# Kernel optimization log

Measured on AMD Instinct MI355X. Metric: run time of the kernel, lower is better.

## Reference

```python
import jax, jax.numpy as jnp
import numpy as np

NMS_PRE, NMS_POST, NMS_THRESH = 1024, 512, 0.7
B, A, FEAT = 4, 70400, 27648
BN_EPS = 1e-5


def _bev_iou(boxes):
    # boxes: [K, 7] (x, y, z, dx, dy, dz, ry); axis-aligned BEV IoU
    x, y, dx, dy = boxes[:, 0], boxes[:, 1], boxes[:, 3], boxes[:, 4]
    x1, x2 = x - 0.5 * dx, x + 0.5 * dx
    y1, y2 = y - 0.5 * dy, y + 0.5 * dy
    iw = jnp.clip(jnp.minimum(x2[:, None], x2[None, :]) - jnp.maximum(x1[:, None], x1[None, :]), 0.0)
    ih = jnp.clip(jnp.minimum(y2[:, None], y2[None, :]) - jnp.maximum(y1[:, None], y1[None, :]), 0.0)
    inter = iw * ih
    area = dx * dy
    return inter / jnp.clip(area[:, None] + area[None, :] - inter, 1e-6)


def _greedy_nms(boxes, thresh):
    # boxes sorted by score desc; returns keep mask [K]
    K = boxes.shape[0]
    iou = _bev_iou(boxes)
    idx = jnp.arange(K)

    def step(keep, i):
        sup = (iou[i] > thresh) & (idx > i) & keep[i]
        return keep & ~sup, None

    keep, _ = jax.lax.scan(step, jnp.ones(K, dtype=bool), jnp.arange(K))
    return keep


def _proposal_one(box, cls):
    # box: [A, 7], cls: [A, n_cls]  ->  padded rois [NPOST,7], scores [NPOST], labels [NPOST]
    score = jnp.max(cls, axis=-1)
    label = jnp.argmax(cls, axis=-1)
    top_score, top_idx = jax.lax.top_k(score, NMS_PRE)
    top_box = box[top_idx]
    keep = _greedy_nms(top_box, NMS_THRESH)
    # stable: kept entries first, preserving score order
    order = jnp.argsort(jnp.where(keep, jnp.arange(NMS_PRE), NMS_PRE + jnp.arange(NMS_PRE)))
    sel = order[:NMS_POST]
    valid = jnp.arange(NMS_POST) < jnp.minimum(jnp.sum(keep), NMS_POST)
    rois = jnp.where(valid[:, None], top_box[sel], 0.0)
    roi_score = jnp.where(valid, top_score[sel], 0.0)
    roi_label = jnp.where(valid, label[top_idx][sel], 0) + 1  # +1 as in module
    return rois, roi_score, roi_label


def _bn_relu(h, g, b):
    # eval-mode BN with running_mean=0, running_var=1
    return jax.nn.relu(h * (g / jnp.sqrt(1.0 + BN_EPS)) + b)


def _decode(reg, anchors):
    # ResidualCoder_v1.decode_torch
    xa, ya, za = anchors[..., 0], anchors[..., 1], anchors[..., 2]
    dxa, dya, dza, ra = anchors[..., 3], anchors[..., 4], anchors[..., 5], anchors[..., 6]
    xt, yt, zt = reg[..., 0], reg[..., 1], reg[..., 2]
    dxt, dyt, dzt, rt = reg[..., 3], reg[..., 4], reg[..., 5], reg[..., 6]
    diag = jnp.sqrt(dxa * dxa + dya * dya)
    return jnp.stack([
        xt * diag + xa, yt * diag + ya, zt * dza + za,
        jnp.exp(dxt) * dxa, jnp.exp(dyt) * dya, jnp.exp(dzt) * dza,
        rt + ra], axis=-1)


def _rotate_z(box, ang):
    # rotate x,y of box [..., 7] by ang [...]
    c, s = jnp.cos(ang), jnp.sin(ang)
    x = box[..., 0] * c - box[..., 1] * s
    y = box[..., 0] * s + box[..., 1] * c
    return jnp.concatenate([x[..., None], y[..., None], box[..., 2:]], axis=-1)


def reference(rpn_box_preds, rpn_cls_preds, pooled_features,
              Ws1, g1, b1, Ws2, g2, b2,
              Wc1, gc1, bc1, Wc2, gc2, bc2, Wc3, bc3,
              Wr1, gr1, br1, Wr2, gr2, br2, Wr3, br3):
    # proposal_layer: per-batch topk + NMS + padded scatter (vmapped)
    rois, roi_scores, roi_labels = jax.vmap(_proposal_one)(rpn_box_preds, rpn_cls_preds)

    # shared / cls / reg heads (1x1 Conv1d == per-roi MLP), dropout off (eval)
    x = _bn_relu(pooled_features @ Ws1.T, g1, b1)
    x = _bn_relu(x @ Ws2.T, g2, b2)
    c = _bn_relu(x @ Wc1.T, gc1, bc1)
    c = _bn_relu(c @ Wc2.T, gc2, bc2)
    cls_preds = c @ Wc3.T + bc3          # [B*NPOST, 1]
    r = _bn_relu(x @ Wr1.T, gr1, br1)
    r = _bn_relu(r @ Wr2.T, gr2, br2)
    reg_preds = r @ Wr3.T + br3          # [B*NPOST, 7]

    bsz = rois.shape[0]
    cls_preds = cls_preds.reshape(bsz, -1, cls_preds.shape[-1])
    reg_preds = reg_preds.reshape(bsz, -1, 7)

    # generate_predict_box: decode against detached rois with xyz zeroed
    anchors = jax.lax.stop_gradient(rois)
    anchors = anchors.at[..., 0:3].set(0.0)
    box_ct = _decode(reg_preds, anchors)
    box_preds = _rotate_z(box_ct, rois[..., 6])
    box_preds = jnp.concatenate([box_preds[..., 0:3] + rois[..., 0:3], box_preds[..., 3:]], axis=-1)

    return jnp.concatenate([cls_preds, box_preds, roi_scores[..., None]], axis=-1)  # [B, NPOST, 9]


def setup_inputs():
    key = jax.random.key(0)
    ks = jax.random.split(key, 32)
    u = jax.random.uniform(ks[0], (B, A, 7), dtype=jnp.float32)
    lo = jnp.array([0.0, -40.0, -2.0, 1.5, 1.4, 1.0, -3.14159], jnp.float32)
    hi = jnp.array([70.0, 40.0, 0.0, 4.5, 2.0, 2.0, 3.14159], jnp.float32)
    rpn_box_preds = lo + u * (hi - lo)
    rpn_cls_preds = jax.random.normal(ks[1], (B, A, 3), dtype=jnp.float32)
    pooled_features = jax.random.normal(ks[2], (B * NMS_POST, FEAT), dtype=jnp.float32) * 0.1

    def w(k, o, i, std=None):
        s = (1.0 / np.sqrt(i)) if std is None else std
        return jax.random.normal(k, (o, i), dtype=jnp.float32) * s

    d = dict(
        rpn_box_preds=rpn_box_preds, rpn_cls_preds=rpn_cls_preds, pooled_features=pooled_features,
        Ws1=w(ks[3], 256, FEAT), g1=jnp.ones(256), b1=jnp.zeros(256),
        Ws2=w(ks[4], 256, 256), g2=jnp.ones(256), b2=jnp.zeros(256),
        Wc1=w(ks[5], 256, 256), gc1=jnp.ones(256), bc1=jnp.zeros(256),
        Wc2=w(ks[6], 256, 256), gc2=jnp.ones(256), bc2=jnp.zeros(256),
        Wc3=w(ks[7], 1, 256), bc3=jnp.zeros(1),
        Wr1=w(ks[8], 256, 256), gr1=jnp.ones(256), br1=jnp.zeros(256),
        Wr2=w(ks[9], 256, 256), gr2=jnp.ones(256), br2=jnp.zeros(256),
        Wr3=w(ks[10], 7, 256, std=0.001), br3=jnp.zeros(7),
    )
    return d
```

## Files before the change

kernel.cpp:

```cpp
#include <hip/hip_runtime.h>
#include <cstdint>

typedef unsigned int u32;
typedef unsigned long long u64;
typedef unsigned short u16;

#define BATCH 4
#define A_CNT 70400
#define FEAT 27648
#define KSPLIT 16
#define KCHUNK 1728
#define NTILE_IT 27

typedef __attribute__((ext_vector_type(8))) short bf16x8;
typedef __attribute__((ext_vector_type(4))) float f32x4;
typedef __attribute__((ext_vector_type(2))) u32 u32x2;
typedef __attribute__((ext_vector_type(4))) u32 u32x4;

constexpr size_t OF_KEYS = 0;
constexpr size_t OF_TBOX = OF_KEYS + 1126400;
constexpr size_t OF_TSC  = OF_TBOX + 114688;
constexpr size_t OF_BX1  = OF_TSC + 16384;
constexpr size_t OF_BX2  = OF_BX1 + 16384;
constexpr size_t OF_BY1  = OF_BX2 + 16384;
constexpr size_t OF_BY2  = OF_BY1 + 16384;
constexpr size_t OF_BAR  = OF_BY2 + 16384;
constexpr size_t OF_MASK = OF_BAR + 16384;
constexpr size_t OF_ROIS = OF_MASK + 524288;
constexpr size_t OF_RSC  = OF_ROIS + 57344;
constexpr size_t OF_BSW  = OF_RSC + 8192;
constexpr size_t OF_PART = OF_BSW + 14155776;
constexpr size_t WS_NEED = OF_PART + 33554432;

__device__ __forceinline__ u32 keyOf(float f) {
  u32 u = __float_as_uint(f);
  return (u & 0x80000000u) ? ~u : (u | 0x80000000u);
}
__device__ __forceinline__ float keyToF(u32 k) {
  u32 u = (k & 0x80000000u) ? (k ^ 0x80000000u) : ~k;
  return __uint_as_float(u);
}
__device__ __forceinline__ u16 f2bf(float f) {
  u32 u = __float_as_uint(f);
  u32 r = 0x7FFFu + ((u >> 16) & 1u);
  return (u16)((u + r) >> 16);
}
__device__ __forceinline__ void gload_lds16(const void* g, void* l) {
  auto gp = reinterpret_cast<const __attribute__((address_space(1))) unsigned int*>(
      reinterpret_cast<uintptr_t>(g));
  auto lp = reinterpret_cast<__attribute__((address_space(3))) unsigned int*>(
      reinterpret_cast<uintptr_t>(l));
  __builtin_amdgcn_global_load_lds(gp, lp, 16, 0, 0);
}
__device__ __forceinline__ u64 shflx64(u64 v, int m) {
  u32 lo = (u32)v, hi = (u32)(v >> 32);
  lo = __shfl_xor(lo, m, 64);
  hi = __shfl_xor(hi, m, 64);
  return ((u64)hi << 32) | lo;
}
__device__ __forceinline__ u32x4 pack8(float4 a, float4 b) {
  u32x4 o;
  o.x = (u32)f2bf(a.x) | ((u32)f2bf(a.y) << 16);
  o.y = (u32)f2bf(a.z) | ((u32)f2bf(a.w) << 16);
  o.z = (u32)f2bf(b.x) | ((u32)f2bf(b.y) << 16);
  o.w = (u32)f2bf(b.z) | ((u32)f2bf(b.w) << 16);
  return o;
}

__global__ __launch_bounds__(1024) void k_fatA(const float* __restrict__ cls,
    const float* __restrict__ Ws1, u32* __restrict__ keys, u32* __restrict__ Bsw)
{
  int bid = blockIdx.x;
  int t = threadIdx.x;
  if (bid < 864) {
    u32 w = (u32)bid * 1024u + t;
    u32 tile = w >> 11;
    u32 rem = w & 2047u;
    u32 n = rem >> 3;
    u32 pq = (rem & 7u) << 4;
    u32 q0 = pq ^ ((n & 7u) << 4);
    u32 col0 = tile * 64u + (q0 >> 1);
    const float* src = Ws1 + (size_t)n * FEAT + col0;
    float4 f0 = *(const float4*)src;
    float4 f1 = *(const float4*)(src + 4);
    ((u32x4*)Bsw)[w] = pack8(f0, f1);
    return;
  }
  u32 g = (u32)(bid - 864) * 1024u + t;
  float s0 = cls[(size_t)g * 3 + 0];
  float s1 = cls[(size_t)g * 3 + 1];
  float s2 = cls[(size_t)g * 3 + 2];
  keys[g] = keyOf(fmaxf(s0, fmaxf(s1, s2)));
}

__global__ __launch_bounds__(1024) void k_big(const u32* __restrict__ keys,
    const float* __restrict__ boxes, const float* __restrict__ A,
    const u32* __restrict__ Bsw, float* __restrict__ part,
    float* __restrict__ tbox, float* __restrict__ tsc,
    float* __restrict__ bx1, float* __restrict__ bx2, float* __restrict__ by1,
    float* __restrict__ by2, float* __restrict__ bar)
{
  __shared__ __align__(16) char smem[131072];
  int bid = blockIdx.x;
  int t = threadIdx.x;
  if (bid < 4) {
    int b = bid;
    int lane = t & 63, wv = t >> 6;
    const u32* kb = keys + (size_t)b * A_CNT;
    u64* s = (u64*)smem;
    u32* partials = (u32*)(smem + 16384);
    u32* ccp = (u32*)(smem + 16448);
    u32 h[35];
#pragma unroll
    for (int j = 0; j < 35; ++j) {
      int g0 = t + ((2 * j) << 10);
      int g1 = t + ((2 * j + 1) << 10);
      u32 a = (g0 < A_CNT) ? (kb[g0] >> 16) : 0u;
      u32 c2 = (g1 < A_CNT) ? (kb[g1] >> 16) : 0u;
      h[j] = a | (c2 << 16);
    }
    if (t == 0) ccp[0] = 0u;
    u32 lo = 0, hi = 65536;
    while (hi - lo > 1) {
      u32 mid = (lo + hi) >> 1;
      u32 c = 0;
#pragma unroll
      for (int j = 0; j < 35; ++j) {
        c += ((h[j] & 0xFFFFu) >= mid) ? 1u : 0u;
        c += ((h[j] >> 16) >= mid) ? 1u : 0u;
      }
#pragma unroll
      for (int o = 32; o > 0; o >>= 1) c += __shfl_xor(c, o, 64);
      __syncthreads();
      if (lane == 0) partials[wv] = c;
      __syncthreads();
      u32 tot = 0;
#pragma unroll
      for (int w2 = 0; w2 < 16; ++w2) tot += partials[w2];
      if (tot >= 1024u) lo = mid; else hi = mid;
    }
    u32 kth = lo;
    __syncthreads();
    u32 kc = kb[t];
#pragma unroll 1
    for (int i = 0; i < 69; ++i) {
      int g = t + (i << 10);
      u32 k = kc;
      if (i < 68) {
        int gn = t + ((i + 1) << 10);
        kc = (gn < A_CNT) ? kb[gn] : 0u;
      }
      bool pass = (g < A_CNT) && ((k >> 16) >= kth);
      u64 mm = __ballot(pass);
      if (mm) {
        int leader = __ffsll((unsigned long long)mm) - 1;
        u32 base = 0;
        if (lane == leader) base = atomicAdd(ccp, (u32)__popcll(mm));
        base = __shfl(base, leader, 64);
        if (pass) {
          u32 pos = base + (u32)__popcll(mm & ((1ull << lane) - 1ull));
          if (pos < 2048u) s[pos] = ((u64)k << 32) | (u32)(~(u32)g);
        }
      }
    }
    __syncthreads();
    u32 m = ccp[0]; if (m > 2048u) m = 2048u;
    for (int e = t; e < 2048; e += 1024) if (e >= (int)m) s[e] = 0ull;
    __syncthreads();
    {
      u64 v0 = s[2 * t], v1 = s[2 * t + 1];
#pragma unroll
      for (u32 k = 2; k <= 128; k <<= 1) {
        bool desc = ((t & (k >> 1)) == 0);
#pragma unroll
        for (u32 j = (k >> 1); j >= 2; j >>= 1) {
          u32 mmk = j >> 1;
          u64 p0 = shflx64(v0, mmk);
          u64 p1 = shflx64(v1, mmk);
          bool up = ((t & mmk) == 0);
          bool mx = (desc == up);
          v0 = mx ? (v0 > p0 ? v0 : p0) : (v0 < p0 ? v0 : p0);
          v1 = mx ? (v1 > p1 ? v1 : p1) : (v1 < p1 ? v1 : p1);
        }
        if (desc ? (v0 < v1) : (v0 > v1)) { u64 tmp = v0; v0 = v1; v1 = tmp; }
      }
      s[2 * t] = v0; s[2 * t + 1] = v1;
      __syncthreads();
      for (u32 k = 256; k <= 2048; k <<= 1) {
        for (u32 j = k >> 1; j >= 128; j >>= 1) {
          for (int e = t; e < 2048; e += 1024) {
            u32 p = (u32)e ^ j;
            if (p > (u32)e) {
              bool d2 = ((e & k) == 0);
              u64 x = s[e], y = s[p];
              if (d2 ? (x < y) : (x > y)) { s[e] = y; s[p] = x; }
            }
          }
          __syncthreads();
        }
        u64 v0 = s[2 * t], v1 = s[2 * t + 1];
        bool desc = ((t & (k >> 1)) == 0);
#pragma unroll
        for (u32 j = 64; j >= 2; j >>= 1) {
          u32 mmk = j >> 1;
          u64 p0 = shflx64(v0, mmk);
          u64 p1 = shflx64(v1, mmk);
          bool up = ((t & mmk) == 0);
          bool mx = (desc == up);
          v0 = mx ? (v0 > p0 ? v0 : p0) : (v0 < p0 ? v0 : p0);
          v1 = mx ? (v1 > p1 ? v1 : p1) : (v1 < p1 ? v1 : p1);
        }
        if (desc ? (v0 < v1) : (v0 > v1)) { u64 tmp = v0; v0 = v1; v1 = tmp; }
        s[2 * t] = v0; s[2 * t + 1] = v1;
        __syncthreads();
      }
    }
    u64 comp = s[t];
    u32 kk = (u32)(comp >> 32);
    u32 a = ~(u32)(comp & 0xFFFFFFFFull);
    int o = b * 1024 + t;
    tsc[o] = keyToF(kk);
    const float* bp = boxes + ((size_t)b * A_CNT + a) * 7;
    float x = bp[0], y = bp[1], z = bp[2], dx = bp[3], dy = bp[4], dz = bp[5], rr = bp[6];
    float* tb = tbox + (size_t)o * 7;
    tb[0] = x; tb[1] = y; tb[2] = z; tb[3] = dx; tb[4] = dy; tb[5] = dz; tb[6] = rr;
    {
#pragma clang fp contract(off)
      bx1[o] = x - 0.5f * dx; bx2[o] = x + 0.5f * dx;
      by1[o] = y - 0.5f * dy; by2[o] = y + 0.5f * dy;
      bar[o] = dx * dy;
    }
    return;
  }
  int bid2 = bid - 4;
  int q = bid2 >> 3;
  int ks = (bid2 & 7) * 2 + (q >> 4);
  int mt = q & 15;
  int lane = t & 63, wvid = t >> 6;
  int row16 = lane & 15, kgrp = lane >> 4;
  int gm = wvid >> 2, gn = wvid & 3;

  f32x4 acc[2][4];
#pragma unroll
  for (int i = 0; i < 2; ++i)
#pragma unroll
    for (int j = 0; j < 4; ++j) acc[i][j] = (f32x4){0.f, 0.f, 0.f, 0.f};

  int arow = t >> 3;
  const float* ap_base = A + ((size_t)(mt * 128 + arow)) * FEAT + (size_t)ks * KCHUNK + (t & 7) * 8;
  int asw = (arow & 7) << 4;
  int awoff = arow * 128 + (((t & 7) * 16) ^ asw);
  const char* bsrc_base = (const char*)Bsw + ((size_t)(ks * NTILE_IT)) * 32768 + wvid * 2048 + lane * 16;
  int bdoff = wvid * 2048 + lane * 16;
  char* Abase = smem;
  char* Bbase = smem + 32768;

  int aoff[2][2], boff[4][2];
#pragma unroll
  for (int ksub = 0; ksub < 2; ++ksub) {
    int qq = ksub * 64 + kgrp * 16;
#pragma unroll
    for (int mf = 0; mf < 2; ++mf) {
      int row = gm * 32 + mf * 16 + row16;
      aoff[mf][ksub] = row * 128 + (qq ^ ((row & 7) << 4));
    }
#pragma unroll
    for (int nf = 0; nf < 4; ++nf) {
      int n = gn * 64 + nf * 16 + row16;
      boff[nf][ksub] = n * 128 + (qq ^ ((n & 7) << 4));
    }
  }

  float4 gaold0, gaold1;
  {
    const float4* ap0 = (const float4*)ap_base;
    float4 a00 = ap0[0], a01 = ap0[1];
    gload_lds16(bsrc_base, Bbase + bdoff);
    gload_lds16(bsrc_base + 1024, Bbase + bdoff + 1024);
    const float4* ap1 = (const float4*)(ap_base + 64);
    gaold0 = ap1[0]; gaold1 = ap1[1];
    const char* bs1 = bsrc_base + 32768;
    gload_lds16(bs1, Bbase + 32768 + bdoff);
    gload_lds16(bs1 + 1024, Bbase + 32768 + bdoff + 1024);
    *(u32x4*)(Abase + awoff) = pack8(a00, a01);
    asm volatile("s_waitcnt lgkmcnt(0)" ::: "memory");
    asm volatile("s_waitcnt vmcnt(4)" ::: "memory");
    __builtin_amdgcn_sched_barrier(0);
    __builtin_amdgcn_s_barrier();
  }

#pragma unroll 1
  for (int it = 0; it < NTILE_IT; ++it) {
    char* Acur = Abase + ((it & 1) << 14);
    char* Bcur = Bbase + (it % 3) * 32768;
    bool pf = (it + 2 < NTILE_IT);
    float4 gn0, gn1;
    if (pf) {
      const float4* ap = (const float4*)(ap_base + (it + 2) * 64);
      gn0 = ap[0]; gn1 = ap[1];
      const char* bs = bsrc_base + (size_t)(it + 2) * 32768;
      char* Bn = Bbase + ((it + 2) % 3) * 32768;
      gload_lds16(bs, Bn + bdoff);
      gload_lds16(bs + 1024, Bn + bdoff + 1024);
    }
    bf16x8 af[2][2], bf[4][2];
#pragma unroll
    for (int ksub = 0; ksub < 2; ++ksub) {
#pragma unroll
      for (int mf = 0; mf < 2; ++mf) af[mf][ksub] = *(const bf16x8*)(Acur + aoff[mf][ksub]);
#pragma unroll
      for (int nf = 0; nf < 4; ++nf) bf[nf][ksub] = *(const bf16x8*)(Bcur + boff[nf][ksub]);
    }
#pragma unroll
    for (int ksub = 0; ksub < 2; ++ksub)
#pragma unroll
      for (int mf = 0; mf < 2; ++mf)
#pragma unroll
        for (int nf = 0; nf < 4; ++nf)
          acc[mf][nf] = __builtin_amdgcn_mfma_f32_16x16x32_bf16(af[mf][ksub], bf[nf][ksub], acc[mf][nf], 0, 0, 0);
    if (it + 1 < NTILE_IT) {
      char* An = Abase + (((it + 1) & 1) << 14);
      *(u32x4*)(An + awoff) = pack8(gaold0, gaold1);
      gaold0 = gn0; gaold1 = gn1;
      asm volatile("s_waitcnt lgkmcnt(0)" ::: "memory");
      if (pf) asm volatile("s_waitcnt vmcnt(4)" ::: "memory");
      else    asm volatile("s_waitcnt vmcnt(0)" ::: "memory");
      __builtin_amdgcn_sched_barrier(0);
      __builtin_amdgcn_s_barrier();
    }
  }
  float* pb = part + (size_t)ks * 524288;
#pragma unroll
  for (int mf = 0; mf < 2; ++mf) {
    int orow = mt * 128 + gm * 32 + mf * 16 + kgrp * 4;
#pragma unroll
    for (int nf = 0; nf < 4; ++nf) {
      int col = gn * 64 + nf * 16 + row16;
#pragma unroll
      for (int rr = 0; rr < 4; ++rr)
        pb[(size_t)(orow + rr) * 256 + col] = acc[mf][nf][rr];
    }
  }
}

__global__ __launch_bounds__(1024) void k_mask(const float* __restrict__ bx1,
    const float* __restrict__ bx2, const float* __restrict__ by1,
    const float* __restrict__ by2, const float* __restrict__ bar,
    u32* __restrict__ mask)
{
  __shared__ float csm[16][5][64];
  int tt = threadIdx.x;
  int ug = tt >> 6, ln = tt & 63;
  int unit = blockIdx.x * 16 + ug;
  int b = unit >> 8, cbk = (unit >> 4) & 15, rb = unit & 15;
  int o = b * 1024, jc0 = cbk * 64;
  int r = rb * 64 + ln;
  csm[ug][0][ln] = bx1[o + jc0 + ln];
  csm[ug][1][ln] = bx2[o + jc0 + ln];
  csm[ug][2][ln] = by1[o + jc0 + ln];
  csm[ug][3][ln] = by2[o + jc0 + ln];
  csm[ug][4][ln] = bar[o + jc0 + ln];
  __syncthreads();
  float rx1 = bx1[o + r], rx2 = bx2[o + r], ry1 = by1[o + r], ry2 = by2[o + r], rar = bar[o + r];
  u32 w0 = 0, w1 = 0;
  {
#pragma clang fp contract(off)
    for (int c = 0; c < 64; ++c) {
      int jc = jc0 + c;
      float iw = fminf(rx2, csm[ug][1][c]) - fmaxf(rx1, csm[ug][0][c]); iw = fmaxf(iw, 0.0f);
      float ih = fminf(ry2, csm[ug][3][c]) - fmaxf(ry1, csm[ug][2][c]); ih = fmaxf(ih, 0.0f);
      float inter = iw * ih;
      float den = fmaxf(rar + csm[ug][4][c] - inter, 1e-6f);
      float iou = inter / den;
      if ((iou > 0.7f) && (jc > r)) {
        if (c < 32) w0 |= 1u << c; else w1 |= 1u << (c - 32);
      }
    }
  }
  mask[((size_t)(o + r)) * 32 + cbk * 2 + 0] = w0;
  mask[((size_t)(o + r)) * 32 + cbk * 2 + 1] = w1;
}

#define CHUNK_STEP(CUR, NXT, C) do {                                            \
    if ((C) + 1 < 32) {                                                         \
      int nb = ((C) + 1) * 1024 + el;                                           \
      _Pragma("unroll")                                                         \
      for (int i = 0; i < 32; ++i) NXT[i] = M[(size_t)(nb + i * 32)];           \
    }                                                                           \
    u32 w = R;                                                                  \
    _Pragma("unroll")                                                           \
    for (int i = 0; i < 32; ++i) w |= ((w >> i) & 1u) ? 0u : CUR[i];            \
    u32 wfin = __shfl(w, (C), 64);                                              \
    u32 m0 = 0, m1 = 0, m2 = 0, m3 = 0;                                         \
    _Pragma("unroll")                                                           \
    for (int i = 0; i < 32; i += 4) {                                           \
      m0 |= ((wfin >> (i + 0)) & 1u) ? 0u : CUR[i + 0];                         \
      m1 |= ((wfin >> (i + 1)) & 1u) ? 0u : CUR[i + 1];                         \
      m2 |= ((wfin >> (i + 2)) & 1u) ? 0u : CUR[i + 2];                         \
      m3 |= ((wfin >> (i + 3)) & 1u) ? 0u : CUR[i + 3];                         \
    }                                                                           \
    R |= (m0 | m1) | (m2 | m3);                                                 \
  } while (0)

__global__ __launch_bounds__(64) void k_nms(const u32* __restrict__ mask,
    const float* __restrict__ tbox, const float* __restrict__ tsc,
    float* __restrict__ rois, float* __restrict__ rsc)
{
  int b = blockIdx.x;
  int lane = threadIdx.x;
  int el = lane & 31;
  const u32* M = mask + (size_t)b * 1024 * 32;
  u32 R = 0;
  u32 bufA[32], bufB[32];
#pragma unroll
  for (int i = 0; i < 32; ++i) bufA[i] = M[(size_t)(i * 32 + el)];
#pragma unroll 1
  for (int c = 0; c < 32; c += 2) {
    CHUNK_STEP(bufA, bufB, c);
    CHUNK_STEP(bufB, bufA, c + 1);
  }
  u32 keepw = (lane < 32) ? ~R : 0u;
  int c = __popc(keepw);
  int pre = c;
  for (int d = 1; d < 64; d <<= 1) {
    int v = __shfl_up(pre, d, 64);
    if (lane >= d) pre += v;
  }
  int total = __shfl(pre, 31, 64);
  int base = pre - c;
  if (lane < 32) {
    u32 w = keepw;
    int rank = base;
    while (w) {
      int bit = __ffs(w) - 1;
      w &= w - 1;
      if (rank < 512) {
        int r = lane * 32 + bit;
        const float* tb = tbox + ((size_t)b * 1024 + r) * 7;
        float* rp = rois + ((size_t)b * 512 + rank) * 7;
        rp[0] = tb[0]; rp[1] = tb[1]; rp[2] = tb[2]; rp[3] = tb[3];
        rp[4] = tb[4]; rp[5] = tb[5]; rp[6] = tb[6];
        rsc[b * 512 + rank] = tsc[b * 1024 + r];
      }
      rank++;
    }
  }
  for (int z = total + lane; z < 512; z += 64) {
    float* rp = rois + ((size_t)b * 512 + z) * 7;
    rp[0] = rp[1] = rp[2] = rp[3] = rp[4] = rp[5] = rp[6] = 0.0f;
    rsc[b * 512 + z] = 0.0f;
  }
}

__device__ __forceinline__ void layer4(const float (*IN)[256], const float* __restrict__ W,
    const float* __restrict__ g, const float* __restrict__ bb, float (*OUT)[256], int t, int h)
{
  float acc[4] = {0, 0, 0, 0};
  const float* Wrow = W + (size_t)t * 256;
  for (int k = 0; k < 256; k += 4) {
    float4 w4 = *(const float4*)&Wrow[k];
#pragma unroll
    for (int r = 0; r < 4; ++r) {
      float4 xv = *(const float4*)&IN[h * 4 + r][k];
      acc[r] = fmaf(xv.x, w4.x, acc[r]);
      acc[r] = fmaf(xv.y, w4.y, acc[r]);
      acc[r] = fmaf(xv.z, w4.z, acc[r]);
      acc[r] = fmaf(xv.w, w4.w, acc[r]);
    }
  }
  float sc = g[t] / sqrtf(1.0f + 1e-5f);
  float bv = bb[t];
#pragma unroll
  for (int r = 0; r < 4; ++r)
    OUT[h * 4 + r][t] = fmaxf(fmaf(acc[r], sc, bv), 0.0f);
}

__global__ __launch_bounds__(512) void k_chain(const float* __restrict__ part,
    const float* __restrict__ Ws2, const float* __restrict__ Wc1, const float* __restrict__ Wc2,
    const float* __restrict__ Wr1, const float* __restrict__ Wr2,
    const float* __restrict__ g1, const float* __restrict__ b1,
    const float* __restrict__ g2, const float* __restrict__ b2,
    const float* __restrict__ gc1, const float* __restrict__ bc1,
    const float* __restrict__ gc2, const float* __restrict__ bc2,
    const float* __restrict__ gr1, const float* __restrict__ br1,
    const float* __restrict__ gr2, const float* __restrict__ br2,
    const float* __restrict__ Wc3, const float* __restrict__ bc3,
    const float* __restrict__ Wr3, const float* __restrict__ br3,
    const float* __restrict__ rois, const float* __restrict__ rsc,
    float* __restrict__ out)
{
  int bid = blockIdx.x, tid = threadIdx.x;
  int t = tid & 255, h = tid >> 8;
  __shared__ __align__(16) float bufX[8][256];
  __shared__ __align__(16) float bufY[8][256];
  __shared__ __align__(16) float bufC[8][256];
  __shared__ __align__(16) float bufR[8][256];
  __shared__ float hd[64];
  {
    float sc = g1[t] / sqrtf(1.0f + 1e-5f);
    float bv = b1[t];
#pragma unroll
    for (int r = 0; r < 4; ++r) {
      int row = h * 4 + r;
      float s = 0.f;
#pragma unroll
      for (int ks = 0; ks < KSPLIT; ++ks)
        s += part[(size_t)ks * 524288 + (size_t)(bid * 8 + row) * 256 + t];
      bufX[row][t] = fmaxf(fmaf(s, sc, bv), 0.0f);
    }
  }
  __syncthreads();
  layer4(bufX, Ws2, g2, b2, bufY, t, h);
  __syncthreads();
  layer4(bufY, Wc1, gc1, bc1, bufC, t, h);
  layer4(bufY, Wr1, gr1, br1, bufR, t, h);
  __syncthreads();
  layer4(bufC, Wc2, gc2, bc2, bufX, t, h);
  layer4(bufR, Wr2, gr2, br2, bufY, t, h);
  __syncthreads();
  int wv = tid >> 6, ln = tid & 63;
  for (int task = wv; task < 64; task += 8) {
    float p;
    if (task < 8) {
      float4 yv = *(const float4*)&bufX[task][ln * 4];
      float4 w4 = ((const float4*)Wc3)[ln];
      p = yv.x * w4.x + yv.y * w4.y + yv.z * w4.z + yv.w * w4.w;
    } else {
      int i = task - 8, row = i / 7, j = i % 7;
      float4 yv = *(const float4*)&bufY[row][ln * 4];
      float4 w4 = ((const float4*)(Wr3 + j * 256))[ln];
      p = yv.x * w4.x + yv.y * w4.y + yv.z * w4.z + yv.w * w4.w;
    }
#pragma unroll
    for (int off = 32; off > 0; off >>= 1) p += __shfl_xor(p, off, 64);
    if (ln == 0) hd[task] = p;
  }
  __syncthreads();
  if (tid < 8) {
    int m = bid * 8 + tid;
    float clsv = hd[tid] + bc3[0];
    float rg[7];
#pragma unroll
    for (int j = 0; j < 7; ++j) rg[j] = hd[8 + tid * 7 + j] + br3[j];
    const float* R = rois + (size_t)m * 7;
    float rx = R[0], ry = R[1], rz = R[2], dxa = R[3], dya = R[4], dza = R[5], ra = R[6];
    float diag = sqrtf(dxa * dxa + dya * dya);
    float x = rg[0] * diag, y = rg[1] * diag, z = rg[2] * dza;
    float ex = expf(rg[3]) * dxa, ey = expf(rg[4]) * dya, ez = expf(rg[5]) * dza;
    float hr = rg[6] + ra;
    float cc = cosf(ra), sn = sinf(ra);
    float xr = x * cc - y * sn, yr = x * sn + y * cc;
    float* O = out + (size_t)m * 9;
    O[0] = clsv; O[1] = xr + rx; O[2] = yr + ry; O[3] = z + rz;
    O[4] = ex; O[5] = ey; O[6] = ez; O[7] = hr; O[8] = rsc[m];
  }
}

extern "C" void kernel_launch(void* const* d_in, const int* in_sizes, int n_in,
                              void* d_out, int out_size, void* d_ws, size_t ws_size,
                              hipStream_t stream)
{
  const float* rpn_box = (const float*)d_in[0];
  const float* rpn_cls = (const float*)d_in[1];
  const float* pooled  = (const float*)d_in[2];
  const float* Ws1 = (const float*)d_in[3];
  const float* g1  = (const float*)d_in[4];
  const float* b1  = (const float*)d_in[5];
  const float* Ws2 = (const float*)d_in[6];
  const float* g2  = (const float*)d_in[7];
  const float* b2  = (const float*)d_in[8];
  const float* Wc1 = (const float*)d_in[9];
  const float* gc1 = (const float*)d_in[10];
  const float* bc1 = (const float*)d_in[11];
  const float* Wc2 = (const float*)d_in[12];
  const float* gc2 = (const float*)d_in[13];
  const float* bc2 = (const float*)d_in[14];
  const float* Wc3 = (const float*)d_in[15];
  const float* bc3 = (const float*)d_in[16];
  const float* Wr1 = (const float*)d_in[17];
  const float* gr1 = (const float*)d_in[18];
  const float* br1 = (const float*)d_in[19];
  const float* Wr2 = (const float*)d_in[20];
  const float* gr2 = (const float*)d_in[21];
  const float* br2 = (const float*)d_in[22];
  const float* Wr3 = (const float*)d_in[23];
  const float* br3 = (const float*)d_in[24];

  if (ws_size < WS_NEED) return;

  char* ws = (char*)d_ws;
  u32* keys = (u32*)(ws + OF_KEYS);
  float* tbox = (float*)(ws + OF_TBOX);
  float* tsc  = (float*)(ws + OF_TSC);
  float* bx1 = (float*)(ws + OF_BX1);
  float* bx2 = (float*)(ws + OF_BX2);
  float* by1 = (float*)(ws + OF_BY1);
  float* by2 = (float*)(ws + OF_BY2);
  float* bar = (float*)(ws + OF_BAR);
  u32* mask = (u32*)(ws + OF_MASK);
  float* roisb = (float*)(ws + OF_ROIS);
  float* rscb  = (float*)(ws + OF_RSC);
  u32* Bsw = (u32*)(ws + OF_BSW);
  float* part = (float*)(ws + OF_PART);

  k_fatA<<<1139, 1024, 0, stream>>>(rpn_cls, Ws1, keys, Bsw);
  k_big<<<260, 1024, 0, stream>>>(keys, rpn_box, pooled, Bsw, part,
                                  tbox, tsc, bx1, bx2, by1, by2, bar);
  k_mask<<<64, 1024, 0, stream>>>(bx1, bx2, by1, by2, bar, mask);
  k_nms<<<4, 64, 0, stream>>>(mask, tbox, tsc, roisb, rscb);
  k_chain<<<256, 512, 0, stream>>>(part, Ws2, Wc1, Wc2, Wr1, Wr2,
                                   g1, b1, g2, b2, gc1, bc1, gc2, bc2,
                                   gr1, br1, gr2, br2, Wc3, bc3, Wr3, br3,
                                   roisb, rscb, (float*)d_out);
}
```

Measured before the change: 242.7 us.

## Halve GEMM k-tile to 32 to cut LDS footprint to 64KB

The split-K GEMM main loop now steps through K in tiles of 32 instead of 64. The loop runs twice as many iterations with one MFMA k-step each, and the A and B staging buffers shrink so shared memory drops from 128KB to 64KB. B tiles are fetched by half from the existing swizzled layout, with unswizzled LDS offsets. The smaller footprint may let two blocks share a CU, at the cost of twice as many barriers and waits per unit of work and shallower prefetch in bytes.

Measured after the change: 282.0 us. 1.16x slower.

```diff
diff --git a/kernel.cpp b/kernel.cpp
--- a/kernel.cpp
+++ b/kernel.cpp
@@ -10,7 +10,7 @@
 #define FEAT 27648
 #define KSPLIT 16
 #define KCHUNK 1728
-#define NTILE_IT 27
+#define NTILE32 54
 
 typedef __attribute__((ext_vector_type(8))) short bf16x8;
 typedef __attribute__((ext_vector_type(4))) float f32x4;
@@ -64,6 +64,12 @@
   o.y = (u32)f2bf(a.z) | ((u32)f2bf(a.w) << 16);
   o.z = (u32)f2bf(b.x) | ((u32)f2bf(b.y) << 16);
   o.w = (u32)f2bf(b.z) | ((u32)f2bf(b.w) << 16);
+  return o;
+}
+__device__ __forceinline__ u32x2 pack4(float4 a) {
+  u32x2 o;
+  o.x = (u32)f2bf(a.x) | ((u32)f2bf(a.y) << 16);
+  o.y = (u32)f2bf(a.z) | ((u32)f2bf(a.w) << 16);
   return o;
 }
 
@@ -100,7 +106,7 @@
     float* __restrict__ bx1, float* __restrict__ bx2, float* __restrict__ by1,
     float* __restrict__ by2, float* __restrict__ bar)
 {
-  __shared__ __align__(16) char smem[131072];
+  __shared__ __align__(16) char smem[65536];
   int bid = blockIdx.x;
   int t = threadIdx.x;
   if (bid < 4) {
@@ -247,83 +253,70 @@
     for (int j = 0; j < 4; ++j) acc[i][j] = (f32x4){0.f, 0.f, 0.f, 0.f};
 
   int arow = t >> 3;
-  const float* ap_base = A + ((size_t)(mt * 128 + arow)) * FEAT + (size_t)ks * KCHUNK + (t & 7) * 8;
-  int asw = (arow & 7) << 4;
-  int awoff = arow * 128 + (((t & 7) * 16) ^ asw);
-  const char* bsrc_base = (const char*)Bsw + ((size_t)(ks * NTILE_IT)) * 32768 + wvid * 2048 + lane * 16;
-  int bdoff = wvid * 2048 + lane * 16;
+  const float* ap_base = A + ((size_t)(mt * 128 + arow)) * FEAT + (size_t)ks * KCHUNK + (t & 7) * 4;
+  int awoff = arow * 64 + (t & 7) * 8;
+  int bn = wvid * 16 + (lane >> 2);
+  int bqp = (lane & 2) ? ((lane & 1) ? 48 : 32) : ((lane & 1) ? 16 : 0);
+  int bsrc_off0 = bn * 128 + (bqp ^ ((bn & 7) << 4));
+  const char* btile_base = (const char*)Bsw + (size_t)(ks * 27) * 32768;
+  int bdst = wvid * 1024 + (lane & 63) * 16;
   char* Abase = smem;
-  char* Bbase = smem + 32768;
-
-  int aoff[2][2], boff[4][2];
-#pragma unroll
-  for (int ksub = 0; ksub < 2; ++ksub) {
-    int qq = ksub * 64 + kgrp * 16;
-#pragma unroll
-    for (int mf = 0; mf < 2; ++mf) {
-      int row = gm * 32 + mf * 16 + row16;
-      aoff[mf][ksub] = row * 128 + (qq ^ ((row & 7) << 4));
-    }
-#pragma unroll
-    for (int nf = 0; nf < 4; ++nf) {
-      int n = gn * 64 + nf * 16 + row16;
-      boff[nf][ksub] = n * 128 + (qq ^ ((n & 7) << 4));
-    }
-  }
-
-  float4 gaold0, gaold1;
+  char* Bbase = smem + 16384;
+
+  int aoff[2], boff[4];
+#pragma unroll
+  for (int mf = 0; mf < 2; ++mf) {
+    int row = gm * 32 + mf * 16 + row16;
+    aoff[mf] = row * 64 + kgrp * 16;
+  }
+#pragma unroll
+  for (int nf = 0; nf < 4; ++nf) {
+    int n = gn * 64 + nf * 16 + row16;
+    boff[nf] = n * 64 + kgrp * 16;
+  }
+
+  float4 gaold;
   {
-    const float4* ap0 = (const float4*)ap_base;
-    float4 a00 = ap0[0], a01 = ap0[1];
-    gload_lds16(bsrc_base, Bbase + bdoff);
-    gload_lds16(bsrc_base + 1024, Bbase + bdoff + 1024);
-    const float4* ap1 = (const float4*)(ap_base + 64);
-    gaold0 = ap1[0]; gaold1 = ap1[1];
-    const char* bs1 = bsrc_base + 32768;
-    gload_lds16(bs1, Bbase + 32768 + bdoff);
-    gload_lds16(bs1 + 1024, Bbase + 32768 + bdoff + 1024);
-    *(u32x4*)(Abase + awoff) = pack8(a00, a01);
+    float4 a0 = *(const float4*)ap_base;
+    gload_lds16(btile_base + bsrc_off0, Bbase + bdst);
+    gaold = *(const float4*)(ap_base + 32);
+    gload_lds16(btile_base + (bsrc_off0 ^ 64), Bbase + 16384 + bdst);
+    *(u32x2*)(Abase + awoff) = pack4(a0);
     asm volatile("s_waitcnt lgkmcnt(0)" ::: "memory");
-    asm volatile("s_waitcnt vmcnt(4)" ::: "memory");
+    asm volatile("s_waitcnt vmcnt(2)" ::: "memory");
     __builtin_amdgcn_sched_barrier(0);
     __builtin_amdgcn_s_barrier();
   }
 
 #pragma unroll 1
-  for (int it = 0; it < NTILE_IT; ++it) {
-    char* Acur = Abase + ((it & 1) << 14);
-    char* Bcur = Bbase + (it % 3) * 32768;
-    bool pf = (it + 2 < NTILE_IT);
-    float4 gn0, gn1;
+  for (int it = 0; it < NTILE32; ++it) {
+    char* Acur = Abase + ((it & 1) << 13);
+    char* Bcur = Bbase + (it % 3) * 16384;
+    bool pf = (it + 2 < NTILE32);
+    float4 gnx;
     if (pf) {
-      const float4* ap = (const float4*)(ap_base + (it + 2) * 64);
-      gn0 = ap[0]; gn1 = ap[1];
-      const char* bs = bsrc_base + (size_t)(it + 2) * 32768;
-      char* Bn = Bbase + ((it + 2) % 3) * 32768;
-      gload_lds16(bs, Bn + bdoff);
-      gload_lds16(bs + 1024, Bn + bdoff + 1024);
-    }
-    bf16x8 af[2][2], bf[4][2];
-#pragma unroll
-    for (int ksub = 0; ksub < 2; ++ksub) {
-#pragma unroll
-      for (int mf = 0; mf < 2; ++mf) af[mf][ksub] = *(const bf16x8*)(Acur + aoff[mf][ksub]);
-#pragma unroll
-      for (int nf = 0; nf < 4; ++nf) bf[nf][ksub] = *(const bf16x8*)(Bcur + boff[nf][ksub]);
-    }
-#pragma unroll
-    for (int ksub = 0; ksub < 2; ++ksub)
-#pragma unroll
-      for (int mf = 0; mf < 2; ++mf)
-#pragma unroll
-        for (int nf = 0; nf < 4; ++nf)
-          acc[mf][nf] = __builtin_amdgcn_mfma_f32_16x16x32_bf16(af[mf][ksub], bf[nf][ksub], acc[mf][nf], 0, 0, 0);
-    if (it + 1 < NTILE_IT) {
-      char* An = Abase + (((it + 1) & 1) << 14);
-      *(u32x4*)(An + awoff) = pack8(gaold0, gaold1);
-      gaold0 = gn0; gaold1 = gn1;
+      gnx = *(const float4*)(ap_base + (it + 2) * 32);
+      int it2 = it + 2;
+      const char* bs = btile_base + (size_t)(it2 >> 1) * 32768;
+      char* Bn = Bbase + (it2 % 3) * 16384;
+      gload_lds16(bs + (bsrc_off0 ^ ((it2 & 1) << 6)), Bn + bdst);
+    }
+    bf16x8 af[2], bf[4];
+#pragma unroll
+    for (int mf = 0; mf < 2; ++mf) af[mf] = *(const bf16x8*)(Acur + aoff[mf]);
+#pragma unroll
+    for (int nf = 0; nf < 4; ++nf) bf[nf] = *(const bf16x8*)(Bcur + boff[nf]);
+#pragma unroll
+    for (int mf = 0; mf < 2; ++mf)
+#pragma unroll
+      for (int nf = 0; nf < 4; ++nf)
+        acc[mf][nf] = __builtin_amdgcn_mfma_f32_16x16x32_bf16(af[mf], bf[nf], acc[mf][nf], 0, 0, 0);
+    if (it + 1 < NTILE32) {
+      char* An = Abase + (((it + 1) & 1) << 13);
+      *(u32x2*)(An + awoff) = pack4(gaold);
+      gaold = gnx;
       asm volatile("s_waitcnt lgkmcnt(0)" ::: "memory");
-      if (pf) asm volatile("s_waitcnt vmcnt(4)" ::: "memory");
+      if (pf) asm volatile("s_waitcnt vmcnt(2)" ::: "memory");
       else    asm volatile("s_waitcnt vmcnt(0)" ::: "memory");
       __builtin_amdgcn_sched_barrier(0);
       __builtin_amdgcn_s_barrier();
```
